# Kernel optimization log

Measured on AMD Instinct MI355X. Metric: run time of the kernel, lower is better.

Reference implementation:

```python
import jax, jax.numpy as jnp
import numpy as np

B, S, D = 2, 2048, 1024
H = 16
DH = D // H  # 64


def setup_inputs() -> dict:
    key = jax.random.key(0)
    k1, k2, k3, k4, k5 = jax.random.split(key, 5)
    scale = 1.0 / np.sqrt(D)
    return {
        "x": jax.random.normal(k1, (B, S, D), dtype=jnp.float32),
        "w_in": jax.random.normal(k2, (3 * D, D), dtype=jnp.float32) * scale,
        "b_in": jax.random.normal(k3, (3 * D,), dtype=jnp.float32) * 0.02,
        "w_out": jax.random.normal(k4, (D, D), dtype=jnp.float32) * scale,
        "b_out": jax.random.normal(k5, (D,), dtype=jnp.float32) * 0.02,
        "mask": 1,
    }


def reference(x, w_in, b_in, w_out, b_out, mask):
    bs, seq_len, d_emb = x.shape
    # in_proj: torch Linear -> x @ W^T + b
    qkv = jnp.einsum("bsd,ed->bse", x, w_in) + b_in  # (B, S, 3D)
    q, k, v = jnp.split(qkv, 3, axis=-1)
    # (B, S, D) -> (B, H, S, DH)
    def heads(t):
        return t.reshape(bs, seq_len, H, DH).transpose(0, 2, 1, 3)
    q, k, v = heads(q), heads(k), heads(v)
    scores = jnp.einsum("bhqd,bhkd->bhqk", q, k)  # (B, H, S, S)
    if mask:
        causal = jnp.triu(jnp.ones((seq_len, seq_len), dtype=bool), k=1)
        scores = jnp.where(causal, -jnp.inf, scores)
    # original divides after masking; -inf / scale is still -inf
    scores = scores / jnp.sqrt(jnp.asarray(DH, dtype=scores.dtype))
    weights = jax.nn.softmax(scores, axis=-1)
    att = jnp.einsum("bhqk,bhkd->bhqd", weights, v)  # (B, H, S, DH)
    att = att.transpose(0, 2, 1, 3).reshape(bs, seq_len, d_emb)
    out = jnp.einsum("bsd,ed->bse", att, w_out) + b_out
    return out
```

## Files before the change

kernel.cpp:

```cpp
#include <hip/hip_runtime.h>
#include <hip/hip_bf16.h>
#include <stdint.h>


typedef __attribute__((ext_vector_type(8))) short bf16x8;
typedef __attribute__((ext_vector_type(4))) float f32x4;
typedef __attribute__((ext_vector_type(16))) float f32x16;
typedef __attribute__((ext_vector_type(4))) unsigned int u32x4;

typedef const __attribute__((address_space(1))) uint32_t* gp1_t;
typedef __attribute__((address_space(3))) uint32_t* lp3_t;

static __device__ __forceinline__ uint32_t cvtpk(float lo, float hi) {
  uint32_t r;
  asm("v_cvt_pk_bf16_f32 %0, %1, %2" : "=v"(r) : "v"(lo), "v"(hi));
  return r;
}
static __device__ __forceinline__ uint16_t f2b(float x) {
  return (uint16_t)cvtpk(x, x);
}
static __device__ __forceinline__ float fexp2(float x) {
  float r;
  asm("v_exp_f32 %0, %1" : "=v"(r) : "v"(x));
  return r;
}

template <int ISSUES>
static __device__ __forceinline__ void stage64(const uint16_t* __restrict__ g, int gstride,
                                               uint8_t* lds, int t) {
#pragma unroll
  for (int i = 0; i < ISSUES; ++i) {
    int p = i * 256 + t;
    int row = p >> 3, c = p & 7;
    const uint16_t* src = g + row * gstride + ((c ^ (row & 7)) << 3);
    __builtin_amdgcn_global_load_lds((gp1_t)src, (lp3_t)(lds + (p & ~63) * 16), 16, 0, 0);
  }
}

static __device__ __forceinline__ bf16x8 ld_frag(const uint8_t* lds, int row, int chunk) {
  return *(const bf16x8*)(lds + row * 128 + (((chunk) ^ (row & 7)) << 4));
}

__global__ __launch_bounds__(256) void cvt3(const float* __restrict__ a,
                                            const float* __restrict__ b,
                                            const float* __restrict__ c,
                                            uint16_t* __restrict__ oa,
                                            uint16_t* __restrict__ ob,
                                            uint16_t* __restrict__ oc) {
  int i = blockIdx.x * 256 + threadIdx.x;
  const float* src;
  uint16_t* dst;
  int j;
  if (i < 1048576)      { src = a; dst = oa; j = i; }
  else if (i < 1835008) { src = b; dst = ob; j = i - 1048576; }
  else                  { src = c; dst = oc; j = i - 1835008; }
  float4 v = ((const float4*)src)[j];
  uint2 o;
  o.x = cvtpk(v.x, v.y);
  o.y = cvtpk(v.z, v.w);
  ((uint2*)dst)[j] = o;
}

__global__ __launch_bounds__(256) void gemm_qkv(const uint16_t* __restrict__ A,
                                                const uint16_t* __restrict__ W,
                                                const float* __restrict__ bias,
                                                uint16_t* __restrict__ Qb,
                                                uint16_t* __restrict__ Kb,
                                                uint16_t* __restrict__ Vt) {
  __shared__ union {
    uint8_t stage[65536];
    uint16_t ot[128][136];
  } sm;
  int t = threadIdx.x, l = t & 63, w = t >> 6;
  int m0 = blockIdx.y * 128, n0 = blockIdx.x * 128;
  int wr = (w >> 1) * 64, wc = (w & 1) * 64;
  const f32x4 fz = {0.f, 0.f, 0.f, 0.f};
  f32x4 acc[4][4];
#pragma unroll
  for (int i = 0; i < 4; ++i)
#pragma unroll
    for (int j = 0; j < 4; ++j) acc[i][j] = fz;

  const uint16_t* Ab_ = A + m0 * 1024;
  const uint16_t* Wb_ = W + n0 * 1024;
  stage64<4>(Ab_, 1024, sm.stage, t);
  stage64<4>(Wb_, 1024, sm.stage + 16384, t);

  for (int kt = 0; kt < 16; ++kt) {
    int cur = kt & 1;
    uint8_t* curb = sm.stage + (cur << 15);
    asm volatile("s_waitcnt vmcnt(0)" ::: "memory");
    __syncthreads();
    if (kt + 1 < 16) {
      uint8_t* nb = sm.stage + ((cur ^ 1) << 15);
      stage64<4>(Ab_ + (kt + 1) * 64, 1024, nb, t);
      stage64<4>(Wb_ + (kt + 1) * 64, 1024, nb + 16384, t);
    }
#pragma unroll
    for (int ks = 0; ks < 2; ++ks) {
      bf16x8 a[4], b[4];
#pragma unroll
      for (int i = 0; i < 4; ++i) {
        a[i] = ld_frag(curb, wr + i * 16 + (l & 15), ks * 4 + (l >> 4));
        b[i] = ld_frag(curb + 16384, wc + i * 16 + (l & 15), ks * 4 + (l >> 4));
      }
#pragma unroll
      for (int i = 0; i < 4; ++i)
#pragma unroll
        for (int j = 0; j < 4; ++j)
          acc[i][j] = __builtin_amdgcn_mfma_f32_16x16x32_bf16(a[i], b[j], acc[i][j], 0, 0, 0);
    }
  }

  __syncthreads();
  const float CSQ = 0.18033688011112042f;
  int sec = n0 >> 10;
#pragma unroll
  for (int j = 0; j < 4; ++j) {
    int col = wc + j * 16 + (l & 15);
    float bv = bias[n0 + col];
#pragma unroll
    for (int i = 0; i < 4; ++i) {
      int rb = wr + i * 16 + ((l >> 4) << 2);
#pragma unroll
      for (int r = 0; r < 4; ++r) {
        int row = rb + r;
        float v = acc[i][j][r] + bv;
        if (sec == 0) v *= CSQ;
        if (sec == 2) {
          int rowp = (row & ~12) | ((row & 4) << 1) | ((row & 8) >> 1);
          sm.ot[col][rowp] = f2b(v);
        } else {
          sm.ot[row][col] = f2b(v);
        }
      }
    }
  }
  __syncthreads();

  int bb0 = m0 >> 11, sbase = m0 & 2047;
  int h0 = (n0 & 1023) >> 6;
  if (sec < 2) {
    uint16_t* dst0 = (sec == 0) ? Qb : Kb;
    int s_loc = t & 127, hh = t >> 7;
    const uint16_t* src = &sm.ot[s_loc][hh * 64];
    uint16_t* dst = dst0 + (((size_t)((bb0 * 16 + h0 + hh) * 2048 + sbase + s_loc)) << 6);
#pragma unroll
    for (int c = 0; c < 8; ++c)
      *(u32x4*)(dst + c * 8) = *(const u32x4*)(src + c * 8);
  } else {
    int re = t >> 1, scc = t & 1;
    int hh = re >> 6, dh = re & 63;
    const uint16_t* src = &sm.ot[re][scc * 64];
    uint16_t* dst = Vt + ((size_t)((bb0 * 16 + h0 + hh) * 64 + dh)) * 2048 + sbase + scc * 64;
#pragma unroll
    for (int c = 0; c < 8; ++c)
      *(u32x4*)(dst + c * 8) = *(const u32x4*)(src + c * 8);
  }
}

__global__ __launch_bounds__(256) void gemm_out(const uint16_t* __restrict__ A,
                                                const uint16_t* __restrict__ W,
                                                const float* __restrict__ bias,
                                                float* __restrict__ out) {
  __shared__ uint8_t sm[65536];
  int t = threadIdx.x, l = t & 63, w = t >> 6;
  int m0 = blockIdx.y * 128, n0 = blockIdx.x * 128;
  int wr = (w >> 1) * 64, wc = (w & 1) * 64;
  const f32x4 fz = {0.f, 0.f, 0.f, 0.f};
  f32x4 acc[4][4];
#pragma unroll
  for (int i = 0; i < 4; ++i)
#pragma unroll
    for (int j = 0; j < 4; ++j) acc[i][j] = fz;

  const uint16_t* Ab_ = A + m0 * 1024;
  const uint16_t* Wb_ = W + n0 * 1024;
  stage64<4>(Ab_, 1024, sm, t);
  stage64<4>(Wb_, 1024, sm + 16384, t);

  for (int kt = 0; kt < 16; ++kt) {
    int cur = kt & 1;
    uint8_t* curb = sm + (cur << 15);
    asm volatile("s_waitcnt vmcnt(0)" ::: "memory");
    __syncthreads();
    if (kt + 1 < 16) {
      uint8_t* nb = sm + ((cur ^ 1) << 15);
      stage64<4>(Ab_ + (kt + 1) * 64, 1024, nb, t);
      stage64<4>(Wb_ + (kt + 1) * 64, 1024, nb + 16384, t);
    }
#pragma unroll
    for (int ks = 0; ks < 2; ++ks) {
      bf16x8 a[4], b[4];
#pragma unroll
      for (int i = 0; i < 4; ++i) {
        a[i] = ld_frag(curb, wr + i * 16 + (l & 15), ks * 4 + (l >> 4));
        b[i] = ld_frag(curb + 16384, wc + i * 16 + (l & 15), ks * 4 + (l >> 4));
      }
#pragma unroll
      for (int i = 0; i < 4; ++i)
#pragma unroll
        for (int j = 0; j < 4; ++j)
          acc[i][j] = __builtin_amdgcn_mfma_f32_16x16x32_bf16(a[i], b[j], acc[i][j], 0, 0, 0);
    }
  }
#pragma unroll
  for (int j = 0; j < 4; ++j) {
    int e = n0 + wc + j * 16 + (l & 15);
    float bv = bias[e];
#pragma unroll
    for (int i = 0; i < 4; ++i) {
      int mb = m0 + wr + i * 16 + ((l >> 4) << 2);
#pragma unroll
      for (int r = 0; r < 4; ++r) {
        int m = mb + r;
        out[m * 1024 + e] = acc[i][j][r] + bv;
      }
    }
  }
}

__global__ __launch_bounds__(512) void attn(const uint16_t* __restrict__ Qb,
                                            const uint16_t* __restrict__ Kb,
                                            const uint16_t* __restrict__ Vt,
                                            uint16_t* __restrict__ Ab,
                                            const int* __restrict__ maskp) {
  __shared__ uint8_t smem[65536];
  int t = threadIdx.x, l = t & 63, w = t >> 6;
  int hi = l >> 5, ql = l & 31;
  int g = w >> 2, wg = w & 3;
  int tl = t & 255;
  int did = (int)blockIdx.x;
  int xcd = did & 7, idx = did >> 3;
  int st = 15 - (idx >> 2);
  int bh = xcd * 4 + (idx & 3);
  bool causal = (*maskp != 0);
  int rounds = causal ? (st + 1) : 16;
  int tile0 = g * rounds;
  int q0w = st * 128 + wg * 32;
  int q = q0w + ql;
  int bb = bh >> 4, h = bh & 15;

  const uint16_t* KpB = Kb + ((size_t)bh << 17);
  const uint16_t* VpB = Vt + ((size_t)bh << 17);
  uint8_t* gbuf = smem + (g << 15);

  bf16x8 qf[4];
  const uint16_t* Qp = Qb + (((size_t)bh * 2048 + q) << 6) + hi * 8;
#pragma unroll
  for (int ks = 0; ks < 4; ++ks) qf[ks] = *(const bf16x8*)(Qp + ks * 16);

  f32x16 acco[2];
#pragma unroll
  for (int r = 0; r < 16; ++r) { acco[0][r] = 0.f; acco[1][r] = 0.f; }
  float lsum = 0.f;

  stage64<2>(KpB + ((size_t)tile0 << 12), 64, gbuf, tl);
  stage64<2>(VpB + tile0 * 64, 2048, gbuf + 8192, tl);

  for (int rr = 0; rr < rounds; ++rr) {
    int tt = tile0 + rr;
    int cur = rr & 1;
    asm volatile("s_waitcnt vmcnt(0)" ::: "memory");
    __syncthreads();
    if (rr + 1 < rounds) {
      uint8_t* nb = gbuf + ((cur ^ 1) << 14);
      stage64<2>(KpB + ((size_t)(tt + 1) << 12), 64, nb, tl);
      stage64<2>(VpB + (tt + 1) * 64, 2048, nb + 8192, tl);
    }
    if (causal && tt * 64 > q0w + 31) continue;

    const uint8_t* Ks = gbuf + (cur << 14);
    const uint8_t* Vs = Ks + 8192;
    bf16x8 kf[2][4], vf[2][4];
#pragma unroll
    for (int ks = 0; ks < 4; ++ks) {
      kf[0][ks] = ld_frag(Ks, ql,      ks * 2 + hi);
      kf[1][ks] = ld_frag(Ks, 32 + ql, ks * 2 + hi);
      vf[0][ks] = ld_frag(Vs, ql,      ks * 2 + hi);
      vf[1][ks] = ld_frag(Vs, 32 + ql, ks * 2 + hi);
    }

    f32x16 sc[2];
#pragma unroll
    for (int r = 0; r < 16; ++r) { sc[0][r] = 0.f; sc[1][r] = 0.f; }
    __builtin_amdgcn_s_setprio(1);
#pragma unroll
    for (int ks = 0; ks < 4; ++ks)
      sc[0] = __builtin_amdgcn_mfma_f32_32x32x16_bf16(kf[0][ks], qf[ks], sc[0], 0, 0, 0);
#pragma unroll
    for (int ks = 0; ks < 4; ++ks)
      sc[1] = __builtin_amdgcn_mfma_f32_32x32x16_bf16(kf[1][ks], qf[ks], sc[1], 0, 0, 0);
    __builtin_amdgcn_s_setprio(0);

    bool nomask = (!causal) || (tt * 64 + 63 <= q0w);
    int qrel = q - tt * 64;
    float rs0 = 0.f, rs1 = 0.f, rs2 = 0.f, rs3 = 0.f;

#pragma unroll
    for (int r = 0; r < 16; ++r) {
      float v = sc[0][r];
      if (!nomask) {
        int kv = (r & 3) + 8 * (r >> 2) + 4 * hi;
        v = (kv <= qrel) ? v : -1e30f;
      }
      float e = fexp2(v);
      sc[0][r] = e;
      if (r & 1) rs1 += e; else rs0 += e;
    }

    __builtin_amdgcn_s_setprio(1);
#pragma unroll
    for (int ks = 0; ks < 2; ++ks) {
      int a8 = ks * 8;
      u32x4 wv = {cvtpk(sc[0][a8 + 0], sc[0][a8 + 1]),
                  cvtpk(sc[0][a8 + 2], sc[0][a8 + 3]),
                  cvtpk(sc[0][a8 + 4], sc[0][a8 + 5]),
                  cvtpk(sc[0][a8 + 6], sc[0][a8 + 7])};
      bf16x8 af = __builtin_bit_cast(bf16x8, wv);
      acco[0] = __builtin_amdgcn_mfma_f32_32x32x16_bf16(af, vf[0][ks], acco[0], 0, 0, 0);
      acco[1] = __builtin_amdgcn_mfma_f32_32x32x16_bf16(af, vf[1][ks], acco[1], 0, 0, 0);
    }
    __builtin_amdgcn_s_setprio(0);

#pragma unroll
    for (int r = 0; r < 16; ++r) {
      float v = sc[1][r];
      if (!nomask) {
        int kv = 32 + (r & 3) + 8 * (r >> 2) + 4 * hi;
        v = (kv <= qrel) ? v : -1e30f;
      }
      float e = fexp2(v);
      sc[1][r] = e;
      if (r & 1) rs3 += e; else rs2 += e;
    }

    __builtin_amdgcn_s_setprio(1);
#pragma unroll
    for (int ks = 0; ks < 2; ++ks) {
      int a8 = ks * 8;
      u32x4 wv = {cvtpk(sc[1][a8 + 0], sc[1][a8 + 1]),
                  cvtpk(sc[1][a8 + 2], sc[1][a8 + 3]),
                  cvtpk(sc[1][a8 + 4], sc[1][a8 + 5]),
                  cvtpk(sc[1][a8 + 6], sc[1][a8 + 7])};
      bf16x8 af = __builtin_bit_cast(bf16x8, wv);
      acco[0] = __builtin_amdgcn_mfma_f32_32x32x16_bf16(af, vf[0][ks + 2], acco[0], 0, 0, 0);
      acco[1] = __builtin_amdgcn_mfma_f32_32x32x16_bf16(af, vf[1][ks + 2], acco[1], 0, 0, 0);
    }
    __builtin_amdgcn_s_setprio(0);

    lsum += (rs0 + rs1) + (rs2 + rs3);
  }

  __syncthreads();
  lsum += __shfl_xor(lsum, 32);
  float (*oaccS)[64][33] = (float(*)[64][33])smem;
  float (*lsumS)[64]     = (float(*)[64])(smem + 33792);
  if (g == 1) {
#pragma unroll
    for (int r = 0; r < 16; ++r) {
      oaccS[wg][l][r] = acco[0][r];
      oaccS[wg][l][16 + r] = acco[1][r];
    }
    lsumS[wg][l] = lsum;
  }
  __syncthreads();
  if (g == 0) {
#pragma unroll
    for (int r = 0; r < 16; ++r) {
      acco[0][r] += oaccS[wg][l][r];
      acco[1][r] += oaccS[wg][l][16 + r];
    }
    lsum += lsumS[wg][l];
#pragma unroll
    for (int r = 0; r < 16; ++r) {
      int crow = (r & 3) + 8 * (r >> 2) + 4 * hi;
      float L = __shfl(lsum, crow);
      float inv = 1.0f / L;
      int qg = q0w + crow;
#pragma unroll
      for (int n = 0; n < 2; ++n)
        Ab[(((size_t)(bb * 2048 + qg)) << 10) + h * 64 + n * 32 + ql] = f2b(acco[n][r] * inv);
    }
  }
}

extern "C" void kernel_launch(void* const* d_in, const int* in_sizes, int n_in,
                              void* d_out, int out_size, void* d_ws, size_t ws_size,
                              hipStream_t stream) {
  const float* x     = (const float*)d_in[0];
  const float* w_in  = (const float*)d_in[1];
  const float* b_in  = (const float*)d_in[2];
  const float* w_out = (const float*)d_in[3];
  const float* b_out = (const float*)d_in[4];
  const int*   mask  = (const int*)d_in[5];
  float* out = (float*)d_out;

  uint8_t* ws = (uint8_t*)d_ws;
  uint16_t* xb  = (uint16_t*)(ws);
  uint16_t* wib = (uint16_t*)(ws + (8u << 20));
  uint16_t* wob = (uint16_t*)(ws + (14u << 20));
  uint16_t* Qb  = (uint16_t*)(ws + (16u << 20));
  uint16_t* Kb  = (uint16_t*)(ws + (24u << 20));
  uint16_t* Vt  = (uint16_t*)(ws + (32u << 20));
  uint16_t* Ab  = (uint16_t*)(ws + (40u << 20));

  cvt3<<<8192, 256, 0, stream>>>(x, w_in, w_out, xb, wib, wob);
  gemm_qkv<<<dim3(24, 32), 256, 0, stream>>>(xb, wib, b_in, Qb, Kb, Vt);
  attn<<<512, 512, 0, stream>>>(Qb, Kb, Vt, Ab, mask);
  gemm_out<<<dim3(8, 32), 256, 0, stream>>>(Ab, wob, b_out, out);
}
```

Measured before the change: 115.7 us.

## Use 128x64 GEMM tiles with XCD-aware block remapping for QKV and out-proj

Halves the N tile of both projection GEMMs from 128 to 64, doubling the grid (1536 and 512 blocks) so the 256 CUs get more and better-balanced work, and shrinks LDS to 48KB. Adds a block-id swizzle that assigns contiguous tiles to each of the 8 XCDs to improve L2 reuse. The epilogue is rewritten for a single head per block. The cost is less operand reuse per block and more redundant A-tile loads.

New measurement: 112.1 us. 3.1% less time.

```diff
diff --git a/kernel.cpp b/kernel.cpp
--- a/kernel.cpp
+++ b/kernel.cpp
@@ -67,56 +67,58 @@
                                                 uint16_t* __restrict__ Qb,
                                                 uint16_t* __restrict__ Kb,
                                                 uint16_t* __restrict__ Vt) {
-  __shared__ union {
-    uint8_t stage[65536];
-    uint16_t ot[128][136];
-  } sm;
+  __shared__ uint8_t smraw[49152];
   int t = threadIdx.x, l = t & 63, w = t >> 6;
-  int m0 = blockIdx.y * 128, n0 = blockIdx.x * 128;
-  int wr = (w >> 1) * 64, wc = (w & 1) * 64;
+  int bid = (int)blockIdx.x + 48 * (int)blockIdx.y;
+  int virt = (bid & 7) * 192 + (bid >> 3);
+  int bx = virt % 48, by = virt / 48;
+  int m0 = by * 128, n0 = bx * 64;
+  int wr = (w >> 1) * 64, wc = (w & 1) * 32;
   const f32x4 fz = {0.f, 0.f, 0.f, 0.f};
-  f32x4 acc[4][4];
+  f32x4 acc[4][2];
 #pragma unroll
   for (int i = 0; i < 4; ++i)
 #pragma unroll
-    for (int j = 0; j < 4; ++j) acc[i][j] = fz;
+    for (int j = 0; j < 2; ++j) acc[i][j] = fz;
 
   const uint16_t* Ab_ = A + m0 * 1024;
   const uint16_t* Wb_ = W + n0 * 1024;
-  stage64<4>(Ab_, 1024, sm.stage, t);
-  stage64<4>(Wb_, 1024, sm.stage + 16384, t);
+  stage64<4>(Ab_, 1024, smraw, t);
+  stage64<2>(Wb_, 1024, smraw + 16384, t);
 
   for (int kt = 0; kt < 16; ++kt) {
     int cur = kt & 1;
-    uint8_t* curb = sm.stage + (cur << 15);
+    uint8_t* curb = smraw + cur * 24576;
     asm volatile("s_waitcnt vmcnt(0)" ::: "memory");
     __syncthreads();
     if (kt + 1 < 16) {
-      uint8_t* nb = sm.stage + ((cur ^ 1) << 15);
+      uint8_t* nb = smraw + (cur ^ 1) * 24576;
       stage64<4>(Ab_ + (kt + 1) * 64, 1024, nb, t);
-      stage64<4>(Wb_ + (kt + 1) * 64, 1024, nb + 16384, t);
+      stage64<2>(Wb_ + (kt + 1) * 64, 1024, nb + 16384, t);
     }
 #pragma unroll
     for (int ks = 0; ks < 2; ++ks) {
-      bf16x8 a[4], b[4];
-#pragma unroll
-      for (int i = 0; i < 4; ++i) {
+      bf16x8 a[4], b[2];
+#pragma unroll
+      for (int i = 0; i < 4; ++i)
         a[i] = ld_frag(curb, wr + i * 16 + (l & 15), ks * 4 + (l >> 4));
-        b[i] = ld_frag(curb + 16384, wc + i * 16 + (l & 15), ks * 4 + (l >> 4));
-      }
+#pragma unroll
+      for (int j = 0; j < 2; ++j)
+        b[j] = ld_frag(curb + 16384, wc + j * 16 + (l & 15), ks * 4 + (l >> 4));
 #pragma unroll
       for (int i = 0; i < 4; ++i)
 #pragma unroll
-        for (int j = 0; j < 4; ++j)
+        for (int j = 0; j < 2; ++j)
           acc[i][j] = __builtin_amdgcn_mfma_f32_16x16x32_bf16(a[i], b[j], acc[i][j], 0, 0, 0);
     }
   }
 
   __syncthreads();
+  uint16_t* ot = (uint16_t*)smraw;
   const float CSQ = 0.18033688011112042f;
   int sec = n0 >> 10;
 #pragma unroll
-  for (int j = 0; j < 4; ++j) {
+  for (int j = 0; j < 2; ++j) {
     int col = wc + j * 16 + (l & 15);
     float bv = bias[n0 + col];
 #pragma unroll
@@ -129,9 +131,9 @@
         if (sec == 0) v *= CSQ;
         if (sec == 2) {
           int rowp = (row & ~12) | ((row & 4) << 1) | ((row & 8) >> 1);
-          sm.ot[col][rowp] = f2b(v);
+          ot[col * 136 + rowp] = f2b(v);
         } else {
-          sm.ot[row][col] = f2b(v);
+          ot[row * 72 + col] = f2b(v);
         }
       }
     }
@@ -139,22 +141,21 @@
   __syncthreads();
 
   int bb0 = m0 >> 11, sbase = m0 & 2047;
-  int h0 = (n0 & 1023) >> 6;
+  int h = (n0 & 1023) >> 6;
   if (sec < 2) {
     uint16_t* dst0 = (sec == 0) ? Qb : Kb;
-    int s_loc = t & 127, hh = t >> 7;
-    const uint16_t* src = &sm.ot[s_loc][hh * 64];
-    uint16_t* dst = dst0 + (((size_t)((bb0 * 16 + h0 + hh) * 2048 + sbase + s_loc)) << 6);
-#pragma unroll
-    for (int c = 0; c < 8; ++c)
+    int s_loc = t >> 1, half = t & 1;
+    const uint16_t* src = ot + s_loc * 72 + half * 32;
+    uint16_t* dst = dst0 + (((size_t)((bb0 * 16 + h) * 2048 + sbase + s_loc)) << 6) + half * 32;
+#pragma unroll
+    for (int c = 0; c < 4; ++c)
       *(u32x4*)(dst + c * 8) = *(const u32x4*)(src + c * 8);
   } else {
-    int re = t >> 1, scc = t & 1;
-    int hh = re >> 6, dh = re & 63;
-    const uint16_t* src = &sm.ot[re][scc * 64];
-    uint16_t* dst = Vt + ((size_t)((bb0 * 16 + h0 + hh) * 64 + dh)) * 2048 + sbase + scc * 64;
-#pragma unroll
-    for (int c = 0; c < 8; ++c)
+    int dh = t >> 2, qr = t & 3;
+    const uint16_t* src = ot + dh * 136 + qr * 32;
+    uint16_t* dst = Vt + ((size_t)((bb0 * 16 + h) * 64 + dh)) * 2048 + sbase + qr * 32;
+#pragma unroll
+    for (int c = 0; c < 4; ++c)
       *(u32x4*)(dst + c * 8) = *(const u32x4*)(src + c * 8);
   }
 }
@@ -163,49 +164,53 @@
                                                 const uint16_t* __restrict__ W,
                                                 const float* __restrict__ bias,
                                                 float* __restrict__ out) {
-  __shared__ uint8_t sm[65536];
+  __shared__ uint8_t sm[49152];
   int t = threadIdx.x, l = t & 63, w = t >> 6;
-  int m0 = blockIdx.y * 128, n0 = blockIdx.x * 128;
-  int wr = (w >> 1) * 64, wc = (w & 1) * 64;
+  int bid = (int)blockIdx.x + 16 * (int)blockIdx.y;
+  int virt = (bid & 7) * 64 + (bid >> 3);
+  int bx = virt % 16, by = virt / 16;
+  int m0 = by * 128, n0 = bx * 64;
+  int wr = (w >> 1) * 64, wc = (w & 1) * 32;
   const f32x4 fz = {0.f, 0.f, 0.f, 0.f};
-  f32x4 acc[4][4];
+  f32x4 acc[4][2];
 #pragma unroll
   for (int i = 0; i < 4; ++i)
 #pragma unroll
-    for (int j = 0; j < 4; ++j) acc[i][j] = fz;
+    for (int j = 0; j < 2; ++j) acc[i][j] = fz;
 
   const uint16_t* Ab_ = A + m0 * 1024;
   const uint16_t* Wb_ = W + n0 * 1024;
   stage64<4>(Ab_, 1024, sm, t);
-  stage64<4>(Wb_, 1024, sm + 16384, t);
+  stage64<2>(Wb_, 1024, sm + 16384, t);
 
   for (int kt = 0; kt < 16; ++kt) {
     int cur = kt & 1;
-    uint8_t* curb = sm + (cur << 15);
+    uint8_t* curb = sm + cur * 24576;
     asm volatile("s_waitcnt vmcnt(0)" ::: "memory");
     __syncthreads();
     if (kt + 1 < 16) {
-      uint8_t* nb = sm + ((cur ^ 1) << 15);
+      uint8_t* nb = sm + (cur ^ 1) * 24576;
       stage64<4>(Ab_ + (kt + 1) * 64, 1024, nb, t);
-      stage64<4>(Wb_ + (kt + 1) * 64, 1024, nb + 16384, t);
+      stage64<2>(Wb_ + (kt + 1) * 64, 1024, nb + 16384, t);
     }
 #pragma unroll
     for (int ks = 0; ks < 2; ++ks) {
-      bf16x8 a[4], b[4];
-#pragma unroll
-      for (int i = 0; i < 4; ++i) {
+      bf16x8 a[4], b[2];
+#pragma unroll
+      for (int i = 0; i < 4; ++i)
         a[i] = ld_frag(curb, wr + i * 16 + (l & 15), ks * 4 + (l >> 4));
-        b[i] = ld_frag(curb + 16384, wc + i * 16 + (l & 15), ks * 4 + (l >> 4));
-      }
+#pragma unroll
+      for (int j = 0; j < 2; ++j)
+        b[j] = ld_frag(curb + 16384, wc + j * 16 + (l & 15), ks * 4 + (l >> 4));
 #pragma unroll
       for (int i = 0; i < 4; ++i)
 #pragma unroll
-        for (int j = 0; j < 4; ++j)
+        for (int j = 0; j < 2; ++j)
           acc[i][j] = __builtin_amdgcn_mfma_f32_16x16x32_bf16(a[i], b[j], acc[i][j], 0, 0, 0);
     }
   }
 #pragma unroll
-  for (int j = 0; j < 4; ++j) {
+  for (int j = 0; j < 2; ++j) {
     int e = n0 + wc + j * 16 + (l & 15);
     float bv = bias[e];
 #pragma unroll
@@ -406,7 +411,7 @@
   uint16_t* Ab  = (uint16_t*)(ws + (40u << 20));
 
   cvt3<<<8192, 256, 0, stream>>>(x, w_in, w_out, xb, wib, wob);
-  gemm_qkv<<<dim3(24, 32), 256, 0, stream>>>(xb, wib, b_in, Qb, Kb, Vt);
+  gemm_qkv<<<dim3(48, 32), 256, 0, stream>>>(xb, wib, b_in, Qb, Kb, Vt);
   attn<<<512, 512, 0, stream>>>(Qb, Kb, Vt, Ab, mask);
-  gemm_out<<<dim3(8, 32), 256, 0, stream>>>(Ab, wob, b_out, out);
-}
+  gemm_out<<<dim3(16, 32), 256, 0, stream>>>(Ab, wob, b_out, out);
+}
```
